# Performance work log

Measured on AMD Instinct MI355X. Metric: run time of the kernel, lower is better.

## Reference

```python
import jax, jax.numpy as jnp
import numpy as np
import math

B, S, D, H, DFF = 4, 1024, 1024, 16, 4096
DK = D // H
EPS = 1e-5


def setup_inputs() -> dict:
    key = jax.random.key(0)
    ks = jax.random.split(key, 16)
    sc = 0.02
    inp = {
        "x": jax.random.normal(ks[0], (B, S, D), jnp.float32),
        "Wq": jax.random.normal(ks[1], (D, D), jnp.float32) * sc,
        "bq": jnp.zeros((D,), jnp.float32),
        "Wk": jax.random.normal(ks[2], (D, D), jnp.float32) * sc,
        "bk": jnp.zeros((D,), jnp.float32),
        "Wv": jax.random.normal(ks[3], (D, D), jnp.float32) * sc,
        "bv": jnp.zeros((D,), jnp.float32),
        "Wo": jax.random.normal(ks[4], (D, D), jnp.float32) * sc,
        "bo": jnp.zeros((D,), jnp.float32),
        "W1": jax.random.normal(ks[5], (D, DFF), jnp.float32) * sc,
        "b1": jnp.zeros((DFF,), jnp.float32),
        "W2": jax.random.normal(ks[6], (DFF, D), jnp.float32) * sc,
        "b2": jnp.zeros((D,), jnp.float32),
        "g1": jnp.ones((D,), jnp.float32),
        "be1": jnp.zeros((D,), jnp.float32),
        "g2": jnp.ones((D,), jnp.float32),
        "be2": jnp.zeros((D,), jnp.float32),
    }
    return inp


def _layernorm(x, g, b):
    mu = jnp.mean(x, axis=-1, keepdims=True)
    var = jnp.mean(jnp.square(x - mu), axis=-1, keepdims=True)
    return (x - mu) * jax.lax.rsqrt(var + EPS) * g + b


def reference(x, Wq, bq, Wk, bk, Wv, bv, Wo, bo, W1, b1, W2, b2, g1, be1, g2, be2):
    # multi-head self-attention (dropout = identity, eval mode)
    q = (x @ Wq + bq).reshape(B, S, H, DK).transpose(0, 2, 1, 3)  # [B,H,S,DK]
    k = (x @ Wk + bk).reshape(B, S, H, DK).transpose(0, 2, 1, 3)
    v = (x @ Wv + bv).reshape(B, S, H, DK).transpose(0, 2, 1, 3)
    scores = jnp.einsum("bhqd,bhkd->bhqk", q, k) / math.sqrt(DK)
    attn_weights = jax.nn.softmax(scores, axis=-1)
    ctx = jnp.einsum("bhqk,bhkd->bhqd", attn_weights, v)
    ctx = ctx.transpose(0, 2, 1, 3).reshape(B, S, D)
    attn_out = ctx @ Wo + bo
    x = _layernorm(x + attn_out, g1, be1)
    ff = jax.nn.relu(x @ W1 + b1) @ W2 + b2
    x = _layernorm(x + ff, g2, be2)
    return x, attn_weights
```

## Files before the change

kernel.cpp:

```cpp
#include <hip/hip_runtime.h>

typedef unsigned short u16;
typedef __attribute__((ext_vector_type(8))) short bf16x8;
typedef __attribute__((ext_vector_type(4))) float f32x4;

__device__ __forceinline__ u16 f2b(float f) {
  unsigned u = __float_as_uint(f);
  u += 0x7fffu + ((u >> 16) & 1u);
  return (u16)(u >> 16);
}
__device__ __forceinline__ float b2f(u16 v) {
  return __uint_as_float((unsigned)v << 16);
}

__device__ __forceinline__ void gload16(const u16* g, u16* l) {
  __builtin_amdgcn_global_load_lds((__attribute__((address_space(1))) void*)(g),
                                   (__attribute__((address_space(3))) void*)(l), 16, 0, 0);
}

__global__ __launch_bounds__(256) void cast_k(const float* __restrict__ s,
                                              u16* __restrict__ d, int n4) {
  int i = blockIdx.x * 256 + threadIdx.x;
  if (i >= n4) return;
  float4 v = *(const float4*)(s + (size_t)i * 4);
  ushort4 o = make_ushort4(f2b(v.x), f2b(v.y), f2b(v.z), f2b(v.w));
  *(ushort4*)(d + (size_t)i * 4) = o;
}

__global__ __launch_bounds__(256) void transpose_k(const float* __restrict__ src,
                                                   u16* __restrict__ dst,
                                                   int ldsrc, int lddst) {
  __shared__ float t[32][33];
  int c0 = blockIdx.x * 32, r0 = blockIdx.y * 32;
  int tx = threadIdx.x, ty = threadIdx.y;
#pragma unroll
  for (int i = 0; i < 4; ++i)
    t[ty + i * 8][tx] = src[(size_t)(r0 + ty + i * 8) * ldsrc + c0 + tx];
  __syncthreads();
#pragma unroll
  for (int i = 0; i < 4; ++i)
    dst[(size_t)(c0 + ty + i * 8) * lddst + r0 + tx] = f2b(t[tx][ty + i * 8]);
}

__global__ __launch_bounds__(256) void transpose4_k(const float* __restrict__ Wq,
                                                    const float* __restrict__ Wk,
                                                    const float* __restrict__ Wv,
                                                    const float* __restrict__ Wo,
                                                    u16* __restrict__ Wqkvt,
                                                    u16* __restrict__ Wot) {
  __shared__ float t[32][33];
  int z = blockIdx.z;
  const float* src = z == 0 ? Wq : z == 1 ? Wk : z == 2 ? Wv : Wo;
  u16* dst = z < 3 ? Wqkvt + (size_t)z * 1048576 : Wot;
  int c0 = blockIdx.x * 32, r0 = blockIdx.y * 32;
  int tx = threadIdx.x, ty = threadIdx.y;
#pragma unroll
  for (int i = 0; i < 4; ++i)
    t[ty + i * 8][tx] = src[(size_t)(r0 + ty + i * 8) * 1024 + c0 + tx];
  __syncthreads();
#pragma unroll
  for (int i = 0; i < 4; ++i)
    dst[(size_t)(c0 + ty + i * 8) * 1024 + r0 + tx] = f2b(t[tx][ty + i * 8]);
}

__global__ __launch_bounds__(256) void transpose_v_k(const u16* __restrict__ qkv,
                                                     u16* __restrict__ vt) {
  __shared__ u16 t[32][33];
  int z = blockIdx.z;
  int b = z >> 4, h = z & 15;
  int s0 = blockIdx.x * 32, d0 = blockIdx.y * 32;
  int tx = threadIdx.x, ty = threadIdx.y;
  const u16* src = qkv + (size_t)(b * 1024) * 3072 + 2048 + h * 64;
  u16* dst = vt + (size_t)z * 65536;
#pragma unroll
  for (int i = 0; i < 4; ++i)
    t[ty + i * 8][tx] = src[(size_t)(s0 + ty + i * 8) * 3072 + d0 + tx];
  __syncthreads();
#pragma unroll
  for (int i = 0; i < 4; ++i)
    dst[(size_t)(d0 + i * 8 + ty) * 1024 + s0 + tx] = t[tx][ty + i * 8];
}

template <int BN, int BIAS, int RELU, int SB16, int SF32, int RESID>
__global__ __launch_bounds__(256) void gemm_k(
    const u16* __restrict__ Ab, long aHi, long aLo, int lda,
    const u16* __restrict__ Bt, long bHi, long bLo, int ldb,
    float* __restrict__ Cf, u16* __restrict__ Cb,
    long cHi, long cLo, int ldc,
    const float* __restrict__ bias, const float* __restrict__ biasB,
    const float* __restrict__ biasC, const float* __restrict__ resid,
    int K, int ZD) {
  constexpr int NT = BN / 32;
  constexpr int CB = (BN * 64 * 2) / 1024;
  __shared__ __align__(128) u16 As[128 * 64];
  __shared__ __align__(128) u16 Bs[BN * 64];

  const int tid = threadIdx.x;
  const int lane = tid & 63;
  const int wave = tid >> 6;
  const int waveM = wave >> 1, waveN = wave & 1;
  const int quad = lane >> 4, l16 = lane & 15;

  const int zb = blockIdx.z / ZD, zr = blockIdx.z % ZD;
  const long aOff = zb * aHi + zr * aLo;
  const long bOff = zb * bHi + zr * bLo;
  const long cOff = zb * cHi + zr * cLo;

  const int row0 = blockIdx.y * 128;
  const int col0 = blockIdx.x * BN;

  const int lr = lane >> 3;
  const int lc = (lane & 7) * 8;

  f32x4 acc[4][NT] = {};

  for (int k0 = 0; k0 < K; k0 += 64) {
    const u16* Ag = Ab + aOff + (long)row0 * lda + k0;
    const u16* Bg = Bt + bOff + (long)col0 * ldb + k0;
#pragma unroll
    for (int c = 0; c < 4; ++c) {
      int ch = c * 4 + wave;
      gload16(Ag + (long)(ch * 8 + lr) * lda + lc, &As[ch * 512]);
    }
#pragma unroll
    for (int c = 0; c < CB / 4; ++c) {
      int ch = c * 4 + wave;
      gload16(Bg + (long)(ch * 8 + lr) * ldb + lc, &Bs[ch * 512]);
    }
    __syncthreads();

    bf16x8 af[4][2], bfr[NT][2];
#pragma unroll
    for (int mi = 0; mi < 4; ++mi)
#pragma unroll
      for (int ks = 0; ks < 2; ++ks)
        af[mi][ks] = *(const bf16x8*)&As[(waveM * 64 + mi * 16 + l16) * 64 + ks * 32 + quad * 8];
#pragma unroll
    for (int ni = 0; ni < NT; ++ni)
#pragma unroll
      for (int ks = 0; ks < 2; ++ks)
        bfr[ni][ks] = *(const bf16x8*)&Bs[(waveN * (BN / 2) + ni * 16 + l16) * 64 + ks * 32 + quad * 8];
#pragma unroll
    for (int ks = 0; ks < 2; ++ks)
#pragma unroll
      for (int mi = 0; mi < 4; ++mi)
#pragma unroll
        for (int ni = 0; ni < NT; ++ni)
          acc[mi][ni] = __builtin_amdgcn_mfma_f32_16x16x32_bf16(af[mi][ks], bfr[ni][ks], acc[mi][ni], 0, 0, 0);
    __syncthreads();
  }

#pragma unroll
  for (int ni = 0; ni < NT; ++ni) {
    int col = col0 + waveN * (BN / 2) + ni * 16 + l16;
    float bv = 0.f;
    if (BIAS == 1) bv = bias[col];
    if (BIAS == 3) bv = col < 1024 ? bias[col] : (col < 2048 ? biasB[col - 1024] : biasC[col - 2048]);
#pragma unroll
    for (int mi = 0; mi < 4; ++mi) {
#pragma unroll
      for (int r = 0; r < 4; ++r) {
        int row = row0 + waveM * 64 + mi * 16 + quad * 4 + r;
        float v = acc[mi][ni][r] + bv;
        if (RELU) v = fmaxf(v, 0.f);
        long idx = cOff + (long)row * ldc + col;
        if (RESID) v += resid[idx];
        if (SF32) Cf[idx] = v;
        if (SB16) Cb[idx] = f2b(v);
      }
    }
  }
}

__global__ __launch_bounds__(256) void score_softmax_k(const u16* __restrict__ qkvb,
                                                       float* __restrict__ attn,
                                                       u16* __restrict__ expb) {
  __shared__ __align__(128) u16 Bs[256 * 64];
  const int tid = threadIdx.x;
  const int lane = tid & 63;
  const int w = tid >> 6;
  const int quad = lane >> 4, l16 = lane & 15;
  const int lr = lane >> 3, lc = (lane & 7) * 8;

  const int z = blockIdx.y;
  const int b = z >> 4, h = z & 15;
  const u16* Q  = qkvb + (long)b * 3145728 + h * 64;
  const u16* Kt = qkvb + (long)b * 3145728 + 1024 + h * 64;

  const int qrow = blockIdx.x * 64 + w * 16 + l16;
  bf16x8 af[2];
  af[0] = *(const bf16x8*)&Q[(long)qrow * 3072 + quad * 8];
  af[1] = *(const bf16x8*)&Q[(long)qrow * 3072 + 32 + quad * 8];

  unsigned p[4][32];
  float rowpart[4] = {0.f, 0.f, 0.f, 0.f};

#pragma unroll 4
  for (int nc = 0; nc < 4; ++nc) {
#pragma unroll
    for (int c = 0; c < 8; ++c) {
      int ch = c * 4 + w;
      gload16(Kt + (long)(nc * 256 + ch * 8 + lr) * 3072 + lc, &Bs[ch * 512]);
    }
    __syncthreads();
#pragma unroll
    for (int ni = 0; ni < 16; ++ni) {
      bf16x8 b0 = *(const bf16x8*)&Bs[(ni * 16 + l16) * 64 + quad * 8];
      bf16x8 b1 = *(const bf16x8*)&Bs[(ni * 16 + l16) * 64 + 32 + quad * 8];
      f32x4 acc = {};
      acc = __builtin_amdgcn_mfma_f32_16x16x32_bf16(af[0], b0, acc, 0, 0, 0);
      acc = __builtin_amdgcn_mfma_f32_16x16x32_bf16(af[1], b1, acc, 0, 0, 0);
      float e0 = __expf(acc[0] * 0.125f);
      float e1 = __expf(acc[1] * 0.125f);
      float e2 = __expf(acc[2] * 0.125f);
      float e3 = __expf(acc[3] * 0.125f);
      rowpart[0] += e0; rowpart[1] += e1; rowpart[2] += e2; rowpart[3] += e3;
      p[nc][ni * 2]     = (unsigned)f2b(e0) | ((unsigned)f2b(e1) << 16);
      p[nc][ni * 2 + 1] = (unsigned)f2b(e2) | ((unsigned)f2b(e3) << 16);
    }
    __syncthreads();
  }

#pragma unroll
  for (int d = 1; d < 16; d <<= 1) {
#pragma unroll
    for (int r = 0; r < 4; ++r) rowpart[r] += __shfl_xor(rowpart[r], d);
  }
  float inv0 = 1.f / rowpart[0], inv1 = 1.f / rowpart[1];
  float inv2 = 1.f / rowpart[2], inv3 = 1.f / rowpart[3];

  const long rbase = (long)z * 1048576 + (long)(blockIdx.x * 64 + w * 16 + quad * 4) * 1024;
#pragma unroll 4
  for (int nc = 0; nc < 4; ++nc) {
#pragma unroll
    for (int ni = 0; ni < 16; ++ni) {
      int col = nc * 256 + ni * 16 + l16;
      unsigned w0 = p[nc][ni * 2], w1 = p[nc][ni * 2 + 1];
      float e0 = b2f((u16)(w0 & 0xffff)) * inv0;
      float e1 = b2f((u16)(w0 >> 16)) * inv1;
      float e2 = b2f((u16)(w1 & 0xffff)) * inv2;
      float e3 = b2f((u16)(w1 >> 16)) * inv3;
      attn[rbase + col] = e0;
      attn[rbase + 1024 + col] = e1;
      attn[rbase + 2048 + col] = e2;
      attn[rbase + 3072 + col] = e3;
      expb[rbase + col] = f2b(e0);
      expb[rbase + 1024 + col] = f2b(e1);
      expb[rbase + 2048 + col] = f2b(e2);
      expb[rbase + 3072 + col] = f2b(e3);
    }
  }
}

template <int WB16, int ADD>
__global__ __launch_bounds__(256) void add_ln_k(const float* __restrict__ xp,
                                                const float* __restrict__ yp,
                                                const float* __restrict__ g,
                                                const float* __restrict__ bta,
                                                float* __restrict__ of,
                                                u16* __restrict__ ob) {
  long row = blockIdx.x;
  int tid = threadIdx.x;
  float4 v = *(const float4*)(xp + row * 1024 + tid * 4);
  if (ADD) {
    const float4 yv = *(const float4*)(yp + row * 1024 + tid * 4);
    v.x += yv.x; v.y += yv.y; v.z += yv.z; v.w += yv.w;
  }
  float s1 = v.x + v.y + v.z + v.w;
  float s2 = v.x * v.x + v.y * v.y + v.z * v.z + v.w * v.w;
#pragma unroll
  for (int d = 32; d > 0; d >>= 1) {
    s1 += __shfl_xor(s1, d);
    s2 += __shfl_xor(s2, d);
  }
  __shared__ float r1[4], r2[4];
  if ((tid & 63) == 0) { r1[tid >> 6] = s1; r2[tid >> 6] = s2; }
  __syncthreads();
  s1 = r1[0] + r1[1] + r1[2] + r1[3];
  s2 = r2[0] + r2[1] + r2[2] + r2[3];
  float mu = s1 * (1.f / 1024.f);
  float var = s2 * (1.f / 1024.f) - mu * mu;
  float rs = rsqrtf(var + 1e-5f);
  float4 gv = *(const float4*)(g + tid * 4);
  float4 bv = *(const float4*)(bta + tid * 4);
  float4 o;
  o.x = (v.x - mu) * rs * gv.x + bv.x;
  o.y = (v.y - mu) * rs * gv.y + bv.y;
  o.z = (v.z - mu) * rs * gv.z + bv.z;
  o.w = (v.w - mu) * rs * gv.w + bv.w;
  *(float4*)(of + row * 1024 + tid * 4) = o;
  if (WB16) {
    ushort4 ov = make_ushort4(f2b(o.x), f2b(o.y), f2b(o.z), f2b(o.w));
    *(ushort4*)(ob + row * 1024 + tid * 4) = ov;
  }
}

extern "C" void kernel_launch(void* const* d_in, const int* in_sizes, int n_in,
                              void* d_out, int out_size, void* d_ws, size_t ws_size,
                              hipStream_t stream) {
  const float* x   = (const float*)d_in[0];
  const float* Wq  = (const float*)d_in[1];
  const float* bq  = (const float*)d_in[2];
  const float* Wk  = (const float*)d_in[3];
  const float* bk  = (const float*)d_in[4];
  const float* Wv  = (const float*)d_in[5];
  const float* bv  = (const float*)d_in[6];
  const float* Wo  = (const float*)d_in[7];
  const float* bo  = (const float*)d_in[8];
  const float* W1  = (const float*)d_in[9];
  const float* b1  = (const float*)d_in[10];
  const float* W2  = (const float*)d_in[11];
  const float* b2  = (const float*)d_in[12];
  const float* g1  = (const float*)d_in[13];
  const float* be1 = (const float*)d_in[14];
  const float* g2  = (const float*)d_in[15];
  const float* be2 = (const float*)d_in[16];

  float* out = (float*)d_out;
  float* attn = out + 4194304LL;

  char* w = (char*)d_ws;
  size_t off = 0;
  auto alloc = [&](size_t bytes) {
    void* p = w + off;
    off = (off + bytes + 255) & ~(size_t)255;
    return p;
  };
  u16* xb        = (u16*)alloc(8388608);
  u16* Wqkvt     = (u16*)alloc(6291456);
  u16* Wot       = (u16*)alloc(2097152);
  u16* W1t       = (u16*)alloc(8388608);
  u16* W2t       = (u16*)alloc(8388608);
  u16* qkvb      = (u16*)alloc(25165824);
  u16* vtb       = (u16*)alloc(8388608);
  u16* expb      = (u16*)alloc(134217728);
  u16* ctxb      = (u16*)alloc(8388608);
  float* attn_o  = (float*)alloc(16777216);
  float* x1      = (float*)alloc(16777216);
  u16* x1b       = (u16*)alloc(8388608);
  u16* ff1b      = (u16*)alloc(33554432);
  float* ff2     = (float*)alloc(16777216);
  (void)ws_size; (void)in_sizes; (void)n_in; (void)out_size;

  dim3 tb(32, 8);
  cast_k<<<4096, 256, 0, stream>>>(x, xb, 1048576);
  transpose4_k<<<dim3(32, 32, 4), tb, 0, stream>>>(Wq, Wk, Wv, Wo, Wqkvt, Wot);
  transpose_k<<<dim3(128, 32), tb, 0, stream>>>(W1, W1t, 4096, 1024);
  transpose_k<<<dim3(32, 128), tb, 0, stream>>>(W2, W2t, 1024, 4096);

  gemm_k<128, 3, 0, 1, 0, 0><<<dim3(24, 32, 1), 256, 0, stream>>>(
      xb, 0, 0, 1024, Wqkvt, 0, 0, 1024,
      nullptr, qkvb, 0, 0, 3072, bq, bk, bv, nullptr, 1024, 1);

  transpose_v_k<<<dim3(32, 2, 64), tb, 0, stream>>>(qkvb, vtb);

  score_softmax_k<<<dim3(16, 64), 256, 0, stream>>>(qkvb, attn, expb);

  gemm_k<64, 0, 0, 1, 0, 0><<<dim3(1, 8, 64), 256, 0, stream>>>(
      expb, 16777216L, 1048576L, 1024,
      vtb, 1048576L, 65536L, 1024,
      nullptr, ctxb, 1048576L, 64, 1024, nullptr, nullptr, nullptr, nullptr, 1024, 16);

  gemm_k<64, 1, 0, 0, 1, 1><<<dim3(16, 32, 1), 256, 0, stream>>>(
      ctxb, 0, 0, 1024, Wot, 0, 0, 1024,
      attn_o, nullptr, 0, 0, 1024, bo, nullptr, nullptr, x, 1024, 1);

  add_ln_k<1, 0><<<4096, 256, 0, stream>>>(attn_o, nullptr, g1, be1, x1, x1b);

  gemm_k<128, 1, 1, 1, 0, 0><<<dim3(32, 32, 1), 256, 0, stream>>>(
      x1b, 0, 0, 1024, W1t, 0, 0, 1024,
      nullptr, ff1b, 0, 0, 4096, b1, nullptr, nullptr, nullptr, 1024, 1);

  gemm_k<64, 1, 0, 0, 1, 1><<<dim3(16, 32, 1), 256, 0, stream>>>(
      ff1b, 0, 0, 4096, W2t, 0, 0, 4096,
      ff2, nullptr, 0, 0, 1024, b2, nullptr, nullptr, x1, 4096, 1);

  add_ln_k<0, 0><<<4096, 256, 0, stream>>>(ff2, nullptr, g2, be2, out, nullptr);
}
```

Before: 727.0 us.

## Fuse score, softmax and PV into one attention kernel; merge prep kernels

Replaces the separate score/softmax kernel and the batched P·V GEMM with one kernel. It computes scores over 128-key chunks, stages unnormalised bf16 probabilities in LDS, and accumulates context through MFMA using swizzled K/V tiles. This removes the 128MB bf16 probability buffer that was written and read back, and writes attention weights as float4. The four cast and transpose launches are also merged into one prep kernel to cut launch count. The trade-off is heavier register use (the p array is kept) and more LDS and barriers per block.

```diff
diff --git a/kernel.cpp b/kernel.cpp
--- a/kernel.cpp
+++ b/kernel.cpp
@@ -18,21 +18,39 @@
                                    (__attribute__((address_space(3))) void*)(l), 16, 0, 0);
 }
 
-__global__ __launch_bounds__(256) void cast_k(const float* __restrict__ s,
-                                              u16* __restrict__ d, int n4) {
-  int i = blockIdx.x * 256 + threadIdx.x;
-  if (i >= n4) return;
-  float4 v = *(const float4*)(s + (size_t)i * 4);
-  ushort4 o = make_ushort4(f2b(v.x), f2b(v.y), f2b(v.z), f2b(v.w));
-  *(ushort4*)(d + (size_t)i * 4) = o;
-}
-
-__global__ __launch_bounds__(256) void transpose_k(const float* __restrict__ src,
-                                                   u16* __restrict__ dst,
-                                                   int ldsrc, int lddst) {
+__global__ __launch_bounds__(256) void prep_k(const float* __restrict__ x, u16* __restrict__ xb,
+                                              const float* __restrict__ Wq, const float* __restrict__ Wk,
+                                              const float* __restrict__ Wv, const float* __restrict__ Wo,
+                                              const float* __restrict__ W1, const float* __restrict__ W2,
+                                              u16* __restrict__ Wqkvt, u16* __restrict__ Wot,
+                                              u16* __restrict__ W1t, u16* __restrict__ W2t) {
+  int bid = blockIdx.x;
+  if (bid < 4096) {
+    int i = bid * 256 + threadIdx.x;
+    float4 v = *(const float4*)(x + (size_t)i * 4);
+    ushort4 o = make_ushort4(f2b(v.x), f2b(v.y), f2b(v.z), f2b(v.w));
+    *(ushort4*)(xb + (size_t)i * 4) = o;
+    return;
+  }
   __shared__ float t[32][33];
-  int c0 = blockIdx.x * 32, r0 = blockIdx.y * 32;
-  int tx = threadIdx.x, ty = threadIdx.y;
+  int tx = threadIdx.x & 31, ty = threadIdx.x >> 5;
+  const float* src;
+  u16* dst;
+  int bx, by, ldsrc, lddst;
+  int r = bid - 4096;
+  if (r < 4096) {
+    int which = r >> 10, rr = r & 1023;
+    bx = rr & 31; by = rr >> 5; ldsrc = 1024; lddst = 1024;
+    src = which == 0 ? Wq : which == 1 ? Wk : which == 2 ? Wv : Wo;
+    dst = which < 3 ? Wqkvt + (size_t)which * 1048576 : Wot;
+  } else if (r < 8192) {
+    int rr = r - 4096;
+    bx = rr & 127; by = rr >> 7; src = W1; dst = W1t; ldsrc = 4096; lddst = 1024;
+  } else {
+    int rr = r - 8192;
+    bx = rr & 31; by = rr >> 5; src = W2; dst = W2t; ldsrc = 1024; lddst = 4096;
+  }
+  int c0 = bx * 32, r0 = by * 32;
 #pragma unroll
   for (int i = 0; i < 4; ++i)
     t[ty + i * 8][tx] = src[(size_t)(r0 + ty + i * 8) * ldsrc + c0 + tx];
@@ -40,27 +58,6 @@
 #pragma unroll
   for (int i = 0; i < 4; ++i)
     dst[(size_t)(c0 + ty + i * 8) * lddst + r0 + tx] = f2b(t[tx][ty + i * 8]);
-}
-
-__global__ __launch_bounds__(256) void transpose4_k(const float* __restrict__ Wq,
-                                                    const float* __restrict__ Wk,
-                                                    const float* __restrict__ Wv,
-                                                    const float* __restrict__ Wo,
-                                                    u16* __restrict__ Wqkvt,
-                                                    u16* __restrict__ Wot) {
-  __shared__ float t[32][33];
-  int z = blockIdx.z;
-  const float* src = z == 0 ? Wq : z == 1 ? Wk : z == 2 ? Wv : Wo;
-  u16* dst = z < 3 ? Wqkvt + (size_t)z * 1048576 : Wot;
-  int c0 = blockIdx.x * 32, r0 = blockIdx.y * 32;
-  int tx = threadIdx.x, ty = threadIdx.y;
-#pragma unroll
-  for (int i = 0; i < 4; ++i)
-    t[ty + i * 8][tx] = src[(size_t)(r0 + ty + i * 8) * 1024 + c0 + tx];
-  __syncthreads();
-#pragma unroll
-  for (int i = 0; i < 4; ++i)
-    dst[(size_t)(c0 + ty + i * 8) * 1024 + r0 + tx] = f2b(t[tx][ty + i * 8]);
 }
 
 __global__ __launch_bounds__(256) void transpose_v_k(const u16* __restrict__ qkv,
@@ -172,82 +169,126 @@
   }
 }
 
-__global__ __launch_bounds__(256) void score_softmax_k(const u16* __restrict__ qkvb,
-                                                       float* __restrict__ attn,
-                                                       u16* __restrict__ expb) {
-  __shared__ __align__(128) u16 Bs[256 * 64];
+__global__ __launch_bounds__(256) void attn_fused_k(const u16* __restrict__ qkvb,
+                                                    const u16* __restrict__ vtb,
+                                                    float* __restrict__ attn,
+                                                    u16* __restrict__ ctxb) {
+  __shared__ __align__(128) u16 Ks[128 * 64];
+  __shared__ __align__(128) u16 Vs[64 * 128];
+  __shared__ __align__(128) u16 Ps[64 * 136];
+  __shared__ float invs[64];
+
   const int tid = threadIdx.x;
   const int lane = tid & 63;
   const int w = tid >> 6;
   const int quad = lane >> 4, l16 = lane & 15;
-  const int lr = lane >> 3, lc = (lane & 7) * 8;
 
   const int z = blockIdx.y;
   const int b = z >> 4, h = z & 15;
-  const u16* Q  = qkvb + (long)b * 3145728 + h * 64;
   const u16* Kt = qkvb + (long)b * 3145728 + 1024 + h * 64;
-
-  const int qrow = blockIdx.x * 64 + w * 16 + l16;
-  bf16x8 af[2];
-  af[0] = *(const bf16x8*)&Q[(long)qrow * 3072 + quad * 8];
-  af[1] = *(const bf16x8*)&Q[(long)qrow * 3072 + 32 + quad * 8];
-
-  unsigned p[4][32];
-  float rowpart[4] = {0.f, 0.f, 0.f, 0.f};
-
-#pragma unroll 4
-  for (int nc = 0; nc < 4; ++nc) {
-#pragma unroll
-    for (int c = 0; c < 8; ++c) {
+  const u16* Vt = vtb + (long)z * 65536;
+
+  const int qabs = blockIdx.x * 64 + w * 16 + l16;
+  const long qrow = ((long)b * 1024 + qabs) * 3072 + h * 64;
+
+  bf16x8 qf0 = *(const bf16x8*)&qkvb[qrow + quad * 8];
+  bf16x8 qf1 = *(const bf16x8*)&qkvb[qrow + 32 + quad * 8];
+
+  unsigned p[8][8][2];
+  float rowsum = 0.f;
+  f32x4 cacc[4] = {};
+
+  const int klr = lane >> 3;
+  const int klc = 8 * ((lane & 7) ^ (lane >> 3));
+  const int vrow_in = lane >> 4;
+
+#pragma unroll
+  for (int nc = 0; nc < 8; ++nc) {
+#pragma unroll
+    for (int c = 0; c < 4; ++c) {
       int ch = c * 4 + w;
-      gload16(Kt + (long)(nc * 256 + ch * 8 + lr) * 3072 + lc, &Bs[ch * 512]);
+      gload16(Kt + (long)(nc * 128 + ch * 8 + klr) * 3072 + klc, &Ks[ch * 512]);
+    }
+#pragma unroll
+    for (int c = 0; c < 4; ++c) {
+      int ch = c * 4 + w;
+      int vr = ch * 4 + vrow_in;
+      int vc = 8 * ((lane & 15) ^ (vr & 7));
+      gload16(Vt + (long)vr * 1024 + nc * 128 + vc, &Vs[ch * 512]);
     }
     __syncthreads();
-#pragma unroll
-    for (int ni = 0; ni < 16; ++ni) {
-      bf16x8 b0 = *(const bf16x8*)&Bs[(ni * 16 + l16) * 64 + quad * 8];
-      bf16x8 b1 = *(const bf16x8*)&Bs[(ni * 16 + l16) * 64 + 32 + quad * 8];
+
+#pragma unroll
+    for (int mi = 0; mi < 8; ++mi) {
+      int R = mi * 16 + l16;
+      bf16x8 kf0 = *(const bf16x8*)&Ks[R * 64 + 8 * (quad ^ (l16 & 7))];
+      bf16x8 kf1 = *(const bf16x8*)&Ks[R * 64 + 8 * ((4 + quad) ^ (l16 & 7))];
       f32x4 acc = {};
-      acc = __builtin_amdgcn_mfma_f32_16x16x32_bf16(af[0], b0, acc, 0, 0, 0);
-      acc = __builtin_amdgcn_mfma_f32_16x16x32_bf16(af[1], b1, acc, 0, 0, 0);
+      acc = __builtin_amdgcn_mfma_f32_16x16x32_bf16(kf0, qf0, acc, 0, 0, 0);
+      acc = __builtin_amdgcn_mfma_f32_16x16x32_bf16(kf1, qf1, acc, 0, 0, 0);
       float e0 = __expf(acc[0] * 0.125f);
       float e1 = __expf(acc[1] * 0.125f);
       float e2 = __expf(acc[2] * 0.125f);
       float e3 = __expf(acc[3] * 0.125f);
-      rowpart[0] += e0; rowpart[1] += e1; rowpart[2] += e2; rowpart[3] += e3;
-      p[nc][ni * 2]     = (unsigned)f2b(e0) | ((unsigned)f2b(e1) << 16);
-      p[nc][ni * 2 + 1] = (unsigned)f2b(e2) | ((unsigned)f2b(e3) << 16);
+      rowsum += (e0 + e1) + (e2 + e3);
+      unsigned p0 = (unsigned)f2b(e0) | ((unsigned)f2b(e1) << 16);
+      unsigned p1 = (unsigned)f2b(e2) | ((unsigned)f2b(e3) << 16);
+      p[nc][mi][0] = p0;
+      p[nc][mi][1] = p1;
+      *(uint2*)&Ps[(w * 16 + l16) * 136 + mi * 16 + quad * 4] = make_uint2(p0, p1);
     }
     __syncthreads();
-  }
-
-#pragma unroll
-  for (int d = 1; d < 16; d <<= 1) {
-#pragma unroll
-    for (int r = 0; r < 4; ++r) rowpart[r] += __shfl_xor(rowpart[r], d);
-  }
-  float inv0 = 1.f / rowpart[0], inv1 = 1.f / rowpart[1];
-  float inv2 = 1.f / rowpart[2], inv3 = 1.f / rowpart[3];
-
-  const long rbase = (long)z * 1048576 + (long)(blockIdx.x * 64 + w * 16 + quad * 4) * 1024;
-#pragma unroll 4
-  for (int nc = 0; nc < 4; ++nc) {
-#pragma unroll
-    for (int ni = 0; ni < 16; ++ni) {
-      int col = nc * 256 + ni * 16 + l16;
-      unsigned w0 = p[nc][ni * 2], w1 = p[nc][ni * 2 + 1];
-      float e0 = b2f((u16)(w0 & 0xffff)) * inv0;
-      float e1 = b2f((u16)(w0 >> 16)) * inv1;
-      float e2 = b2f((u16)(w1 & 0xffff)) * inv2;
-      float e3 = b2f((u16)(w1 >> 16)) * inv3;
-      attn[rbase + col] = e0;
-      attn[rbase + 1024 + col] = e1;
-      attn[rbase + 2048 + col] = e2;
-      attn[rbase + 3072 + col] = e3;
-      expb[rbase + col] = f2b(e0);
-      expb[rbase + 1024 + col] = f2b(e1);
-      expb[rbase + 2048 + col] = f2b(e2);
-      expb[rbase + 3072 + col] = f2b(e3);
+
+    {
+      int VR = w * 16 + l16;
+#pragma unroll
+      for (int ks = 0; ks < 4; ++ks) {
+        bf16x8 vf = *(const bf16x8*)&Vs[VR * 128 + 8 * ((ks * 4 + quad) ^ (l16 & 7))];
+#pragma unroll
+        for (int ni = 0; ni < 4; ++ni) {
+          bf16x8 pf = *(const bf16x8*)&Ps[(ni * 16 + l16) * 136 + ks * 32 + quad * 8];
+          cacc[ni] = __builtin_amdgcn_mfma_f32_16x16x32_bf16(vf, pf, cacc[ni], 0, 0, 0);
+        }
+      }
+    }
+    __syncthreads();
+  }
+
+  rowsum += __shfl_xor(rowsum, 16);
+  rowsum += __shfl_xor(rowsum, 32);
+  float inv = 1.f / rowsum;
+  if (quad == 0) invs[w * 16 + l16] = inv;
+  __syncthreads();
+
+  u16* ctx_lds = Ks;
+#pragma unroll
+  for (int ni = 0; ni < 4; ++ni) {
+    float iv = invs[ni * 16 + l16];
+    unsigned c01 = (unsigned)f2b(cacc[ni][0] * iv) | ((unsigned)f2b(cacc[ni][1] * iv) << 16);
+    unsigned c23 = (unsigned)f2b(cacc[ni][2] * iv) | ((unsigned)f2b(cacc[ni][3] * iv) << 16);
+    *(uint2*)&ctx_lds[(ni * 16 + l16) * 72 + w * 16 + quad * 4] = make_uint2(c01, c23);
+  }
+  __syncthreads();
+#pragma unroll
+  for (int i = 0; i < 2; ++i) {
+    int q = w * 16 + (lane >> 3) + i * 8;
+    int d0 = (lane & 7) * 8;
+    bf16x8 cv = *(const bf16x8*)&ctx_lds[q * 72 + d0];
+    long tok = (long)b * 1024 + blockIdx.x * 64 + q;
+    *(bf16x8*)&ctxb[tok * 1024 + h * 64 + d0] = cv;
+  }
+
+  const long arow = ((long)z * 1024 + qabs) * 1024;
+#pragma unroll
+  for (int nc = 0; nc < 8; ++nc) {
+#pragma unroll
+    for (int mi = 0; mi < 8; ++mi) {
+      float4 v;
+      v.x = b2f((u16)(p[nc][mi][0] & 0xffff)) * inv;
+      v.y = b2f((u16)(p[nc][mi][0] >> 16)) * inv;
+      v.z = b2f((u16)(p[nc][mi][1] & 0xffff)) * inv;
+      v.w = b2f((u16)(p[nc][mi][1] >> 16)) * inv;
+      *(float4*)&attn[arow + nc * 128 + mi * 16 + quad * 4] = v;
     }
   }
 }
@@ -333,7 +374,6 @@
   u16* W2t       = (u16*)alloc(8388608);
   u16* qkvb      = (u16*)alloc(25165824);
   u16* vtb       = (u16*)alloc(8388608);
-  u16* expb      = (u16*)alloc(134217728);
   u16* ctxb      = (u16*)alloc(8388608);
   float* attn_o  = (float*)alloc(16777216);
   float* x1      = (float*)alloc(16777216);
@@ -342,24 +382,15 @@
   float* ff2     = (float*)alloc(16777216);
   (void)ws_size; (void)in_sizes; (void)n_in; (void)out_size;
 
-  dim3 tb(32, 8);
-  cast_k<<<4096, 256, 0, stream>>>(x, xb, 1048576);
-  transpose4_k<<<dim3(32, 32, 4), tb, 0, stream>>>(Wq, Wk, Wv, Wo, Wqkvt, Wot);
-  transpose_k<<<dim3(128, 32), tb, 0, stream>>>(W1, W1t, 4096, 1024);
-  transpose_k<<<dim3(32, 128), tb, 0, stream>>>(W2, W2t, 1024, 4096);
+  prep_k<<<16384, 256, 0, stream>>>(x, xb, Wq, Wk, Wv, Wo, W1, W2, Wqkvt, Wot, W1t, W2t);
 
   gemm_k<128, 3, 0, 1, 0, 0><<<dim3(24, 32, 1), 256, 0, stream>>>(
       xb, 0, 0, 1024, Wqkvt, 0, 0, 1024,
       nullptr, qkvb, 0, 0, 3072, bq, bk, bv, nullptr, 1024, 1);
 
-  transpose_v_k<<<dim3(32, 2, 64), tb, 0, stream>>>(qkvb, vtb);
-
-  score_softmax_k<<<dim3(16, 64), 256, 0, stream>>>(qkvb, attn, expb);
-
-  gemm_k<64, 0, 0, 1, 0, 0><<<dim3(1, 8, 64), 256, 0, stream>>>(
-      expb, 16777216L, 1048576L, 1024,
-      vtb, 1048576L, 65536L, 1024,
-      nullptr, ctxb, 1048576L, 64, 1024, nullptr, nullptr, nullptr, nullptr, 1024, 16);
+  transpose_v_k<<<dim3(32, 2, 64), dim3(32, 8), 0, stream>>>(qkvb, vtb);
+
+  attn_fused_k<<<dim3(16, 64), 256, 0, stream>>>(qkvb, vtb, attn, ctxb);
 
   gemm_k<64, 1, 0, 0, 1, 1><<<dim3(16, 32, 1), 256, 0, stream>>>(
       ctxb, 0, 0, 1024, Wot, 0, 0, 1024,
```

Measured after the change: 699.9 us. -3.7%, faster.
